# Performance work log

Measured on AMD Instinct MI355X. Metric: run time of the kernel, lower is better.

Reference implementation:

```python
import jax, jax.numpy as jnp
import numpy as np

B, S, D_MODEL = 2, 2048, 2048
H, HKV, HD = 16, 16, 128


def setup_inputs() -> dict:
    key = jax.random.key(0)
    k1, k2, k3, k4, k5 = jax.random.split(key, 5)
    hidden_states = jax.random.normal(k1, (B, S, D_MODEL), dtype=jnp.float32)
    cos = jax.random.uniform(k2, (S, HD), dtype=jnp.float32)
    sin = jax.random.uniform(k3, (S, HD), dtype=jnp.float32)
    W_qkv = jax.random.normal(k4, (D_MODEL, (H + 2 * HKV) * HD), dtype=jnp.float32) * (D_MODEL ** -0.5)
    W_o = jax.random.normal(k5, (H * HD, D_MODEL), dtype=jnp.float32) * ((H * HD) ** -0.5)
    return {"hidden_states": hidden_states, "cos": cos, "sin": sin, "W_qkv": W_qkv, "W_o": W_o}


def _rotate_half(x):
    x1, x2 = jnp.split(x, 2, axis=-1)
    return jnp.concatenate([-x2, x1], axis=-1)


def reference(hidden_states, cos, sin, W_qkv, W_o):
    b, s, _ = hidden_states.shape
    qkv = jnp.einsum('bsd,de->bse', hidden_states, W_qkv)
    qkv = qkv.reshape(b, s, H + 2 * HKV, HD)  # B S (H+2Hkv) D
    q = qkv[:, :, :H]
    k = qkv[:, :, H:H + HKV]
    v = qkv[:, :, H + HKV:]
    # rotary: cos/sin [S, D] broadcast over batch and heads
    c = cos[None, :, None, :]
    sn = sin[None, :, None, :]
    q = q * c + _rotate_half(q) * sn
    k = k * c + _rotate_half(k) * sn
    # B S H D -> B H S D
    q = jnp.transpose(q, (0, 2, 1, 3))
    k = jnp.transpose(k, (0, 2, 1, 3))
    v = jnp.transpose(v, (0, 2, 1, 3))
    scale = HD ** -0.5
    scores = jnp.einsum('bhqd,bhkd->bhqk', q, k) * scale
    attn = jax.nn.softmax(scores.astype(jnp.float32), axis=-1).astype(q.dtype)
    attn = jax.lax.stop_gradient(attn)  # frozen attention pattern (detach)
    out = jnp.einsum('bhqk,bhkd->bhqd', attn, v)
    out = jnp.transpose(out, (0, 2, 1, 3)).reshape(b, s, H * HD)
    return jnp.einsum('bsd,de->bse', out, W_o)
```

## Files before the change

### kernel.cpp

```cpp
#include <hip/hip_runtime.h>

typedef _Float16 f16;
typedef _Float16 half8 __attribute__((ext_vector_type(8)));
typedef _Float16 half4 __attribute__((ext_vector_type(4)));
typedef float f32x4 __attribute__((ext_vector_type(4)));

#define B_ 2
#define S_ 2048
#define DM_ 2048
#define H_ 16
#define HD_ 128
#define EQ_ 6144
#define SCALE_Q 0.08838834764831845f

__global__ void k_cast(const float* __restrict__ in, f16* __restrict__ out, int n4) {
  int i = blockIdx.x * blockDim.x + threadIdx.x;
  int stride = gridDim.x * blockDim.x;
  for (; i < n4; i += stride) {
    float4 v = ((const float4*)in)[i];
    half4 h = { (f16)v.x, (f16)v.y, (f16)v.z, (f16)v.w };
    ((half4*)out)[i] = h;
  }
}

__global__ void k_tcast(const float* __restrict__ in, f16* __restrict__ out, int K, int N) {
  __shared__ float tile[64][65];
  const int t = threadIdx.x;
  const int nb = blockIdx.x * 64, kb = blockIdx.y * 64;
  const int tr = t >> 4, tc4 = (t & 15) * 4;
  #pragma unroll
  for (int i = 0; i < 4; ++i) {
    int k = tr + i * 16;
    float4 v = *(const float4*)&in[(size_t)(kb + k) * N + nb + tc4];
    tile[k][tc4 + 0] = v.x; tile[k][tc4 + 1] = v.y;
    tile[k][tc4 + 2] = v.z; tile[k][tc4 + 3] = v.w;
  }
  __syncthreads();
  #pragma unroll
  for (int i = 0; i < 4; ++i) {
    int n = tr + i * 16;
    half4 h = { (f16)tile[tc4 + 0][n], (f16)tile[tc4 + 1][n],
                (f16)tile[tc4 + 2][n], (f16)tile[tc4 + 3][n] };
    *(half4*)&out[(size_t)(nb + n) * K + kb + tc4] = h;
  }
}

__global__ __launch_bounds__(256, 2) void k_gemm(
    const f16* __restrict__ A, const f16* __restrict__ Bt,
    f16* __restrict__ C16, float* __restrict__ C32,
    int M, int N, int K, int writeF32)
{
  __shared__ __attribute__((aligned(16))) f16 As[128 * 64];
  __shared__ __attribute__((aligned(16))) f16 Bs[128 * 64];
  const int t = threadIdx.x;
  const int lane = t & 63, wave = t >> 6;
  const int lr = lane & 15, hi4 = lane >> 4;
  const int wr = wave >> 1, wc = wave & 1;
  const int row0 = blockIdx.x * 128, col0 = blockIdx.y * 128;

  const int sr = t >> 1;
  const int sc0 = (t & 1) * 4;
  const f16* ga = &A[(size_t)(row0 + sr) * K + sc0 * 8];
  const f16* gb = &Bt[(size_t)(col0 + sr) * K + sc0 * 8];

  half8 ra[4], rb[4];
  #pragma unroll
  for (int i = 0; i < 4; ++i) {
    ra[i] = *(const half8*)(ga + i * 8);
    rb[i] = *(const half8*)(gb + i * 8);
  }

  f32x4 acc[4][4];
  #pragma unroll
  for (int m = 0; m < 4; ++m)
    #pragma unroll
    for (int n = 0; n < 4; ++n)
      acc[m][n] = (f32x4){0.f, 0.f, 0.f, 0.f};

  char* asb = (char*)As;
  char* bsb = (char*)Bs;
  const int nk = K >> 6;
  for (int kt = 0; kt < nk; ++kt) {
    __syncthreads();
    #pragma unroll
    for (int i = 0; i < 4; ++i) {
      int cc = (sc0 + i) ^ (sr & 7);
      *(half8*)(asb + sr * 128 + cc * 16) = ra[i];
      *(half8*)(bsb + sr * 128 + cc * 16) = rb[i];
    }
    __syncthreads();
    if (kt + 1 < nk) {
      #pragma unroll
      for (int i = 0; i < 4; ++i) {
        ra[i] = *(const half8*)(ga + (kt + 1) * 64 + i * 8);
        rb[i] = *(const half8*)(gb + (kt + 1) * 64 + i * 8);
      }
    }
    #pragma unroll
    for (int ks = 0; ks < 2; ++ks) {
      half8 af[4], bf[4];
      #pragma unroll
      for (int m = 0; m < 4; ++m) {
        int ar = wr * 64 + m * 16 + lr;
        af[m] = *(const half8*)(asb + ar * 128 + (((ks * 4 + hi4) ^ (ar & 7)) << 4));
      }
      #pragma unroll
      for (int n = 0; n < 4; ++n) {
        int br = wc * 64 + n * 16 + lr;
        bf[n] = *(const half8*)(bsb + br * 128 + (((ks * 4 + hi4) ^ (br & 7)) << 4));
      }
      #pragma unroll
      for (int m = 0; m < 4; ++m)
        #pragma unroll
        for (int n = 0; n < 4; ++n)
          acc[m][n] = __builtin_amdgcn_mfma_f32_16x16x32_f16(af[m], bf[n], acc[m][n], 0, 0, 0);
    }
  }
  #pragma unroll
  for (int m = 0; m < 4; ++m)
    #pragma unroll
    for (int n = 0; n < 4; ++n)
      #pragma unroll
      for (int j = 0; j < 4; ++j) {
        int row = row0 + wr * 64 + m * 16 + hi4 * 4 + j;
        int col = col0 + wc * 64 + n * 16 + lr;
        if (writeF32) C32[(size_t)row * N + col] = acc[m][n][j];
        else          C16[(size_t)row * N + col] = (f16)acc[m][n][j];
      }
}

__global__ void k_rope(const f16* __restrict__ qkv, const float* __restrict__ cosb,
                       const float* __restrict__ sinb, f16* __restrict__ Qf, f16* __restrict__ Kf)
{
  const int bx = blockIdx.x;
  const int bs = bx >> 4;
  const int h = (bx & 15) * 2 + (threadIdx.x >> 7);
  const int d = threadIdx.x & 127;
  const int s = bs & (S_ - 1);
  const int b = bs >> 11;
  float x  = (float)qkv[(size_t)bs * EQ_ + h * HD_ + d];
  float xp = (float)qkv[(size_t)bs * EQ_ + h * HD_ + (d ^ 64)];
  float sgn = (d < 64) ? -1.0f : 1.0f;
  float v = x * cosb[s * HD_ + d] + sgn * xp * sinb[s * HD_ + d];
  if (h < H_) {
    v *= SCALE_Q;
    Qf[(((size_t)(b * H_ + h)) * S_ + s) * HD_ + d] = (f16)v;
  } else {
    Kf[(((size_t)(b * H_ + (h - H_))) * S_ + s) * HD_ + d] = (f16)v;
  }
}

__global__ void k_vtrans(const f16* __restrict__ qkv, f16* __restrict__ VT)
{
  __shared__ __attribute__((aligned(16))) f16 tile[128][136];
  const int bx = blockIdx.x;
  const int st = bx & 15, h = (bx >> 4) & 15, b = bx >> 8;
  const int t = threadIdx.x;
  const int sl = t >> 1, dc = (t & 1) * 64;
  const int bs = b * S_ + st * 128 + sl;
  #pragma unroll
  for (int i = 0; i < 8; ++i) {
    half8 v = *(const half8*)&qkv[(size_t)bs * EQ_ + (32 + h) * HD_ + dc + i * 8];
    *(half8*)&tile[sl][dc + i * 8] = v;
  }
  __syncthreads();
  const int dr = t >> 1, scc = (t & 1) * 64;
  #pragma unroll
  for (int i = 0; i < 8; ++i) {
    half8 v;
    #pragma unroll
    for (int j = 0; j < 8; ++j) v[j] = tile[scc + i * 8 + j][dr];
    *(half8*)&VT[(((size_t)(b * H_ + h)) * HD_ + dr) * S_ + st * 128 + scc + i * 8] = v;
  }
}

__global__ __launch_bounds__(256, 2) void k_attn(
    const f16* __restrict__ Qf, const f16* __restrict__ Kf, const f16* __restrict__ VT,
    f16* __restrict__ Oout)
{
  __shared__ __attribute__((aligned(16))) char lds[64 * 272 + 128 * 160 + 4 * 32 * 160];
  char* Ks = lds;
  char* Vs = lds + 64 * 272;
  char* Ps = Vs + 128 * 160;
  const int bx = blockIdx.x;
  const int qt = bx & 15, h = (bx >> 4) & 15, b = bx >> 8;
  const int t = threadIdx.x, lane = t & 63, wave = t >> 6;
  const int lr = lane & 15, hi4 = lane >> 4;
  const size_t bh = (size_t)(b * H_ + h);
  const int q0 = qt * 128 + wave * 32;

  half8 qf[2][4];
  #pragma unroll
  for (int m = 0; m < 2; ++m)
    #pragma unroll
    for (int ds = 0; ds < 4; ++ds)
      qf[m][ds] = *(const half8*)&Qf[(bh * S_ + q0 + m * 16 + lr) * HD_ + ds * 32 + hi4 * 8];

  f32x4 o[2][8];
  #pragma unroll
  for (int m = 0; m < 2; ++m)
    #pragma unroll
    for (int dc = 0; dc < 8; ++dc) o[m][dc] = (f32x4){0.f, 0.f, 0.f, 0.f};
  float mstate[2][4], lstate[2][4];
  #pragma unroll
  for (int m = 0; m < 2; ++m)
    #pragma unroll
    for (int j = 0; j < 4; ++j) { mstate[m][j] = -1e30f; lstate[m][j] = 0.f; }

  const int kr = t >> 2;
  const int vr = t >> 1;
  const f16* Kg = &Kf[bh * S_ * HD_];
  const f16* Vg = &VT[bh * HD_ * S_];

  for (int kt = 0; kt < S_ / 64; ++kt) {
    __syncthreads();
    #pragma unroll
    for (int i = 0; i < 4; ++i) {
      int c = (t & 3) + i * 4;
      *(half8*)(Ks + kr * 272 + c * 16) = *(const half8*)&Kg[(size_t)(kt * 64 + kr) * HD_ + c * 8];
    }
    #pragma unroll
    for (int i = 0; i < 4; ++i) {
      int c = (t & 1) + i * 2;
      *(half8*)(Vs + vr * 160 + c * 16) = *(const half8*)&Vg[(size_t)vr * S_ + kt * 64 + c * 8];
    }
    __syncthreads();

    f32x4 sc[2][4];
    #pragma unroll
    for (int m = 0; m < 2; ++m)
      #pragma unroll
      for (int n = 0; n < 4; ++n) sc[m][n] = (f32x4){0.f, 0.f, 0.f, 0.f};
    #pragma unroll
    for (int ds = 0; ds < 4; ++ds) {
      half8 kf[4];
      #pragma unroll
      for (int n = 0; n < 4; ++n)
        kf[n] = *(const half8*)(Ks + (n * 16 + lr) * 272 + ds * 64 + hi4 * 16);
      #pragma unroll
      for (int m = 0; m < 2; ++m)
        #pragma unroll
        for (int n = 0; n < 4; ++n)
          sc[m][n] = __builtin_amdgcn_mfma_f32_16x16x32_f16(qf[m][ds], kf[n], sc[m][n], 0, 0, 0);
    }

    float mx[2][4], corr[2][4], rs[2][4];
    #pragma unroll
    for (int m = 0; m < 2; ++m)
      #pragma unroll
      for (int j = 0; j < 4; ++j)
        mx[m][j] = fmaxf(fmaxf(sc[m][0][j], sc[m][1][j]), fmaxf(sc[m][2][j], sc[m][3][j]));
    #pragma unroll
    for (int mask = 1; mask < 16; mask <<= 1)
      #pragma unroll
      for (int m = 0; m < 2; ++m)
        #pragma unroll
        for (int j = 0; j < 4; ++j)
          mx[m][j] = fmaxf(mx[m][j], __shfl_xor(mx[m][j], mask));
    #pragma unroll
    for (int m = 0; m < 2; ++m)
      #pragma unroll
      for (int j = 0; j < 4; ++j) {
        float nm = fmaxf(mstate[m][j], mx[m][j]);
        corr[m][j] = __expf(mstate[m][j] - nm);
        mstate[m][j] = nm;
        rs[m][j] = 0.f;
      }
    #pragma unroll
    for (int m = 0; m < 2; ++m)
      #pragma unroll
      for (int n = 0; n < 4; ++n)
        #pragma unroll
        for (int j = 0; j < 4; ++j) {
          float p = __expf(sc[m][n][j] - mstate[m][j]);
          sc[m][n][j] = p;
          rs[m][j] += p;
        }
    #pragma unroll
    for (int mask = 1; mask < 16; mask <<= 1)
      #pragma unroll
      for (int m = 0; m < 2; ++m)
        #pragma unroll
        for (int j = 0; j < 4; ++j)
          rs[m][j] += __shfl_xor(rs[m][j], mask);
    #pragma unroll
    for (int m = 0; m < 2; ++m)
      #pragma unroll
      for (int j = 0; j < 4; ++j)
        lstate[m][j] = lstate[m][j] * corr[m][j] + rs[m][j];
    #pragma unroll
    for (int m = 0; m < 2; ++m)
      #pragma unroll
      for (int dc = 0; dc < 8; ++dc)
        #pragma unroll
        for (int j = 0; j < 4; ++j) o[m][dc][j] *= corr[m][j];

    #pragma unroll
    for (int m = 0; m < 2; ++m)
      #pragma unroll
      for (int n = 0; n < 4; ++n)
        #pragma unroll
        for (int j = 0; j < 4; ++j) {
          int prow = wave * 32 + m * 16 + hi4 * 4 + j;
          *(f16*)(Ps + prow * 160 + (n * 16 + lr) * 2) = (f16)sc[m][n][j];
        }
    __syncthreads();

    #pragma unroll
    for (int ks = 0; ks < 2; ++ks) {
      half8 pa[2];
      #pragma unroll
      for (int m = 0; m < 2; ++m)
        pa[m] = *(const half8*)(Ps + (wave * 32 + m * 16 + lr) * 160 + ks * 64 + hi4 * 16);
      #pragma unroll
      for (int dc = 0; dc < 8; ++dc) {
        half8 vb = *(const half8*)(Vs + (dc * 16 + lr) * 160 + ks * 64 + hi4 * 16);
        #pragma unroll
        for (int m = 0; m < 2; ++m)
          o[m][dc] = __builtin_amdgcn_mfma_f32_16x16x32_f16(pa[m], vb, o[m][dc], 0, 0, 0);
      }
    }
  }

  float inv[2][4];
  #pragma unroll
  for (int m = 0; m < 2; ++m)
    #pragma unroll
    for (int j = 0; j < 4; ++j) inv[m][j] = 1.0f / lstate[m][j];
  #pragma unroll
  for (int m = 0; m < 2; ++m)
    #pragma unroll
    for (int dc = 0; dc < 8; ++dc)
      #pragma unroll
      for (int j = 0; j < 4; ++j) {
        int row = b * S_ + qt * 128 + wave * 32 + m * 16 + hi4 * 4 + j;
        int col = h * 128 + dc * 16 + lr;
        Oout[(size_t)row * DM_ + col] = (f16)(o[m][dc][j] * inv[m][j]);
      }
}

extern "C" void kernel_launch(void* const* d_in, const int* in_sizes, int n_in,
                              void* d_out, int out_size, void* d_ws, size_t ws_size,
                              hipStream_t stream) {
  (void)in_sizes; (void)n_in; (void)out_size; (void)ws_size;
  const float* hidden = (const float*)d_in[0];
  const float* cosb   = (const float*)d_in[1];
  const float* sinb   = (const float*)d_in[2];
  const float* W_qkv  = (const float*)d_in[3];
  const float* W_o    = (const float*)d_in[4];
  float* out = (float*)d_out;

  f16* Ah    = (f16*)d_ws;
  f16* Wqt   = Ah    + (size_t)8388608;
  f16* Wot   = Wqt   + (size_t)12582912;
  f16* qkv16 = Wot   + (size_t)4194304;
  f16* Qf    = qkv16 + (size_t)25165824;
  f16* Kf    = Qf    + (size_t)8388608;
  f16* VT    = Kf    + (size_t)8388608;
  f16* AO    = VT    + (size_t)8388608;

  k_cast<<<2048, 256, 0, stream>>>(hidden, Ah, 2097152);
  k_tcast<<<dim3(EQ_ / 64, 2048 / 64), 256, 0, stream>>>(W_qkv, Wqt, 2048, EQ_);
  k_tcast<<<dim3(2048 / 64, 2048 / 64), 256, 0, stream>>>(W_o, Wot, 2048, 2048);
  k_gemm<<<dim3(32, EQ_ / 128), 256, 0, stream>>>(Ah, Wqt, qkv16, nullptr, 4096, EQ_, 2048, 0);
  k_rope<<<B_ * S_ * 16, 256, 0, stream>>>(qkv16, cosb, sinb, Qf, Kf);
  k_vtrans<<<512, 256, 0, stream>>>(qkv16, VT);
  k_attn<<<512, 256, 0, stream>>>(Qf, Kf, VT, AO);
  k_gemm<<<dim3(32, 16), 256, 0, stream>>>(AO, Wot, nullptr, out, 4096, 2048, 2048, 1);
}
```

Measured before the change: 486.3 us.

## Use direct global-to-LDS loads in GEMM, swizzle attention LDS, exp2 softmax

The GEMM now fills shared memory with global_load_lds and drops the register prefetch and XOR swizzle, so its LDS reads become unswizzled and global loads are no longer overlapped with MFMA. The attention kernel replaces padded K/V/P layouts with XOR-swizzled ones and gives each wave a private P tile, which replaces a block barrier with a compiler fence. The softmax folds log2(e) into the Q scale and uses exp2f. Risks include bank conflicts from the unswizzled GEMM reads and serialized load latency in the GEMM.

```diff
diff --git a/kernel.cpp b/kernel.cpp
--- a/kernel.cpp
+++ b/kernel.cpp
@@ -11,7 +11,13 @@
 #define H_ 16
 #define HD_ 128
 #define EQ_ 6144
-#define SCALE_Q 0.08838834764831845f
+#define SCALE_Q (0.08838834764831845f * 1.4426950408889634f)
+
+__device__ __forceinline__ void gload16(const void* g, void* l) {
+  __builtin_amdgcn_global_load_lds(
+      (const __attribute__((address_space(1))) unsigned int*)g,
+      (__attribute__((address_space(3))) unsigned int*)l, 16, 0, 0);
+}
 
 __global__ void k_cast(const float* __restrict__ in, f16* __restrict__ out, int n4) {
   int i = blockIdx.x * blockDim.x + threadIdx.x;
@@ -58,17 +64,11 @@
   const int wr = wave >> 1, wc = wave & 1;
   const int row0 = blockIdx.x * 128, col0 = blockIdx.y * 128;
 
-  const int sr = t >> 1;
-  const int sc0 = (t & 1) * 4;
-  const f16* ga = &A[(size_t)(row0 + sr) * K + sc0 * 8];
-  const f16* gb = &Bt[(size_t)(col0 + sr) * K + sc0 * 8];
-
-  half8 ra[4], rb[4];
-  #pragma unroll
-  for (int i = 0; i < 4; ++i) {
-    ra[i] = *(const half8*)(ga + i * 8);
-    rb[i] = *(const half8*)(gb + i * 8);
-  }
+  const int srow = lane >> 3, schunk = lane & 7;
+  const f16* gA = &A[(size_t)(row0 + wave * 32 + srow) * K + schunk * 8];
+  const f16* gB = &Bt[(size_t)(col0 + wave * 32 + srow) * K + schunk * 8];
+  char* asb = (char*)As;
+  char* bsb = (char*)Bs;
 
   f32x4 acc[4][4];
   #pragma unroll
@@ -77,38 +77,24 @@
     for (int n = 0; n < 4; ++n)
       acc[m][n] = (f32x4){0.f, 0.f, 0.f, 0.f};
 
-  char* asb = (char*)As;
-  char* bsb = (char*)Bs;
   const int nk = K >> 6;
   for (int kt = 0; kt < nk; ++kt) {
     __syncthreads();
     #pragma unroll
     for (int i = 0; i < 4; ++i) {
-      int cc = (sc0 + i) ^ (sr & 7);
-      *(half8*)(asb + sr * 128 + cc * 16) = ra[i];
-      *(half8*)(bsb + sr * 128 + cc * 16) = rb[i];
+      gload16(gA + (size_t)(i * 8) * K + kt * 64, asb + wave * 4096 + i * 1024);
+      gload16(gB + (size_t)(i * 8) * K + kt * 64, bsb + wave * 4096 + i * 1024);
     }
     __syncthreads();
-    if (kt + 1 < nk) {
-      #pragma unroll
-      for (int i = 0; i < 4; ++i) {
-        ra[i] = *(const half8*)(ga + (kt + 1) * 64 + i * 8);
-        rb[i] = *(const half8*)(gb + (kt + 1) * 64 + i * 8);
-      }
-    }
     #pragma unroll
     for (int ks = 0; ks < 2; ++ks) {
       half8 af[4], bf[4];
       #pragma unroll
-      for (int m = 0; m < 4; ++m) {
-        int ar = wr * 64 + m * 16 + lr;
-        af[m] = *(const half8*)(asb + ar * 128 + (((ks * 4 + hi4) ^ (ar & 7)) << 4));
-      }
-      #pragma unroll
-      for (int n = 0; n < 4; ++n) {
-        int br = wc * 64 + n * 16 + lr;
-        bf[n] = *(const half8*)(bsb + br * 128 + (((ks * 4 + hi4) ^ (br & 7)) << 4));
-      }
+      for (int m = 0; m < 4; ++m)
+        af[m] = *(const half8*)(asb + (wr * 64 + m * 16 + lr) * 128 + ks * 64 + hi4 * 16);
+      #pragma unroll
+      for (int n = 0; n < 4; ++n)
+        bf[n] = *(const half8*)(bsb + (wc * 64 + n * 16 + lr) * 128 + ks * 64 + hi4 * 16);
       #pragma unroll
       for (int m = 0; m < 4; ++m)
         #pragma unroll
@@ -127,6 +113,7 @@
         if (writeF32) C32[(size_t)row * N + col] = acc[m][n][j];
         else          C16[(size_t)row * N + col] = (f16)acc[m][n][j];
       }
+  (void)M;
 }
 
 __global__ void k_rope(const f16* __restrict__ qkv, const float* __restrict__ cosb,
@@ -178,14 +165,14 @@
     const f16* __restrict__ Qf, const f16* __restrict__ Kf, const f16* __restrict__ VT,
     f16* __restrict__ Oout)
 {
-  __shared__ __attribute__((aligned(16))) char lds[64 * 272 + 128 * 160 + 4 * 32 * 160];
+  __shared__ __attribute__((aligned(16))) char lds[3 * 16384];
   char* Ks = lds;
-  char* Vs = lds + 64 * 272;
-  char* Ps = Vs + 128 * 160;
+  char* Vs = lds + 16384;
   const int bx = blockIdx.x;
   const int qt = bx & 15, h = (bx >> 4) & 15, b = bx >> 8;
   const int t = threadIdx.x, lane = t & 63, wave = t >> 6;
   const int lr = lane & 15, hi4 = lane >> 4;
+  char* Ps = lds + 32768 + wave * 4096;
   const size_t bh = (size_t)(b * H_ + h);
   const int q0 = qt * 128 + wave * 32;
 
@@ -217,12 +204,14 @@
     #pragma unroll
     for (int i = 0; i < 4; ++i) {
       int c = (t & 3) + i * 4;
-      *(half8*)(Ks + kr * 272 + c * 16) = *(const half8*)&Kg[(size_t)(kt * 64 + kr) * HD_ + c * 8];
+      *(half8*)(Ks + kr * 256 + ((c ^ (kr & 7)) << 4)) =
+          *(const half8*)&Kg[(size_t)(kt * 64 + kr) * HD_ + c * 8];
     }
     #pragma unroll
     for (int i = 0; i < 4; ++i) {
       int c = (t & 1) + i * 2;
-      *(half8*)(Vs + vr * 160 + c * 16) = *(const half8*)&Vg[(size_t)vr * S_ + kt * 64 + c * 8];
+      *(half8*)(Vs + vr * 128 + ((c ^ (vr & 7)) << 4)) =
+          *(const half8*)&Vg[(size_t)vr * S_ + kt * 64 + c * 8];
     }
     __syncthreads();
 
@@ -235,8 +224,10 @@
     for (int ds = 0; ds < 4; ++ds) {
       half8 kf[4];
       #pragma unroll
-      for (int n = 0; n < 4; ++n)
-        kf[n] = *(const half8*)(Ks + (n * 16 + lr) * 272 + ds * 64 + hi4 * 16);
+      for (int n = 0; n < 4; ++n) {
+        int ar = n * 16 + lr;
+        kf[n] = *(const half8*)(Ks + ar * 256 + ((((ds * 4 + hi4) ^ (ar & 7))) << 4));
+      }
       #pragma unroll
       for (int m = 0; m < 2; ++m)
         #pragma unroll
@@ -262,7 +253,7 @@
       #pragma unroll
       for (int j = 0; j < 4; ++j) {
         float nm = fmaxf(mstate[m][j], mx[m][j]);
-        corr[m][j] = __expf(mstate[m][j] - nm);
+        corr[m][j] = exp2f(mstate[m][j] - nm);
         mstate[m][j] = nm;
         rs[m][j] = 0.f;
       }
@@ -272,7 +263,7 @@
       for (int n = 0; n < 4; ++n)
         #pragma unroll
         for (int j = 0; j < 4; ++j) {
-          float p = __expf(sc[m][n][j] - mstate[m][j]);
+          float p = exp2f(sc[m][n][j] - mstate[m][j]);
           sc[m][n][j] = p;
           rs[m][j] += p;
         }
@@ -301,20 +292,23 @@
       for (int n = 0; n < 4; ++n)
         #pragma unroll
         for (int j = 0; j < 4; ++j) {
-          int prow = wave * 32 + m * 16 + hi4 * 4 + j;
-          *(f16*)(Ps + prow * 160 + (n * 16 + lr) * 2) = (f16)sc[m][n][j];
+          int prow = m * 16 + hi4 * 4 + j;
+          *(f16*)(Ps + prow * 128 + ((n * 32 + lr * 2) ^ ((prow & 7) << 4))) = (f16)sc[m][n][j];
         }
-    __syncthreads();
+    asm volatile("" ::: "memory");
 
     #pragma unroll
     for (int ks = 0; ks < 2; ++ks) {
       half8 pa[2];
       #pragma unroll
-      for (int m = 0; m < 2; ++m)
-        pa[m] = *(const half8*)(Ps + (wave * 32 + m * 16 + lr) * 160 + ks * 64 + hi4 * 16);
+      for (int m = 0; m < 2; ++m) {
+        int pr = m * 16 + lr;
+        pa[m] = *(const half8*)(Ps + pr * 128 + ((((ks * 4 + hi4) ^ (pr & 7))) << 4));
+      }
       #pragma unroll
       for (int dc = 0; dc < 8; ++dc) {
-        half8 vb = *(const half8*)(Vs + (dc * 16 + lr) * 160 + ks * 64 + hi4 * 16);
+        int rv = dc * 16 + lr;
+        half8 vb = *(const half8*)(Vs + rv * 128 + ((((ks * 4 + hi4) ^ (rv & 7))) << 4));
         #pragma unroll
         for (int m = 0; m < 2; ++m)
           o[m][dc] = __builtin_amdgcn_mfma_f32_16x16x32_f16(pa[m], vb, o[m][dc], 0, 0, 0);
```

Measured after the change: 543.1 us. 11.7% more time.
